# Optimization experiments

Hardware: AMD Instinct MI355X
Metric: run time of the kernel (lower is better)

Reference implementation:

```python
import jax, jax.numpy as jnp
import numpy as np

EPS = 1e-5

def _bn(x, g, b, m, v):
    # inference-mode batchnorm over channel axis 1
    s = (1, -1) + (1,) * (x.ndim - 2)
    return (x - m.reshape(s)) * (g.reshape(s) / jnp.sqrt(v.reshape(s) + EPS)) + b.reshape(s)

def _lrelu(x):
    return jnp.where(x >= 0, x, 0.2 * x)

def _graph_feature(x, k):
    # x: (B, C, N) -> (B, 2C, N, k): DGCNN cat([neighbor - center, center])
    xt = jnp.transpose(x, (0, 2, 1))                      # (B, N, C)
    sq = jnp.sum(xt * xt, axis=-1)                        # (B, N)
    neg_dist = 2.0 * jnp.einsum('bnc,bmc->bnm', xt, xt) - sq[:, :, None] - sq[:, None, :]
    idx = jax.lax.top_k(neg_dist, k)[1]                   # (B, N, k) nearest (incl. self)
    nb = jax.vmap(lambda f, i: f[i])(xt, idx)             # (B, N, k, C) neighbor gather
    ctr = jnp.broadcast_to(xt[:, :, None, :], nb.shape)
    feat = jnp.concatenate([nb - ctr, ctr], axis=-1)      # (B, N, k, 2C)
    return jnp.transpose(feat, (0, 3, 1, 2))

def _edge_conv(x, k, w, g, b, m, v):
    # 1x1 conv over edge features + BN + LeakyReLU(0.2) + max over k neighbors
    f = _graph_feature(x, k)
    h = jnp.einsum('oi,bink->bonk', w, f)
    return jnp.max(_lrelu(_bn(h, g, b, m, v)), axis=-1)   # (B, out, N)

def setup_inputs():
    key = jax.random.key(0)
    ks = jax.random.split(key, 40)
    rn = lambda i, s: jax.random.normal(ks[i], s, dtype=jnp.float32)
    ru = lambda i, s: jax.random.uniform(ks[i], s, dtype=jnp.float32)
    B, N, K = 8, 1024, 20
    inp = {'x': rn(0, (B, N, 3))}
    dims = [(64, 6), (64, 128), (128, 128), (256, 256)]
    for li, (o, ci) in enumerate(dims, 1):
        base = li * 5
        inp[f'c{li}w'] = rn(base, (o, ci)) * 0.2
        inp[f'c{li}g'] = ru(base + 1, (o,)) + 0.5
        inp[f'c{li}b'] = rn(base + 2, (o,)) * 0.1
        inp[f'c{li}m'] = rn(base + 3, (o,)) * 0.1
        inp[f'c{li}v'] = ru(base + 4, (o,)) + 0.5
    inp['f1w'] = rn(25, (128, 384)) * 0.05
    inp['f1b'] = rn(26, (128,)) * 0.1
    inp['n1g'] = ru(27, (128,)) + 0.5
    inp['n1b'] = rn(28, (128,)) * 0.1
    inp['n1m'] = rn(29, (128,)) * 0.1
    inp['n1v'] = ru(30, (128,)) + 0.5
    inp['f2w'] = rn(31, (16, 128)) * 0.1
    inp['f2b'] = rn(32, (16,)) * 0.1
    inp['n2g'] = ru(33, (16,)) + 0.5
    inp['n2b'] = rn(34, (16,)) * 0.1
    inp['n2m'] = rn(35, (16,)) * 0.1
    inp['n2v'] = ru(36, (16,)) + 0.5
    inp['f3w'] = rn(37, (1, 16)) * 0.2
    inp['f3b'] = rn(38, (1,)) * 0.1
    inp['k'] = K
    return inp

def reference(x, c1w, c1g, c1b, c1m, c1v, c2w, c2g, c2b, c2m, c2v,
              c3w, c3g, c3b, c3m, c3v, c4w, c4g, c4b, c4m, c4v,
              f1w, f1b, n1g, n1b, n1m, n1v, f2w, f2b, n2g, n2b, n2m, n2v,
              f3w, f3b, k):
    xt = jnp.transpose(x, (0, 2, 1))                       # (B, 3, N)
    h1 = _edge_conv(xt, k, c1w, c1g, c1b, c1m, c1v)        # (B, 64, N)
    h2 = _edge_conv(h1, k, c2w, c2g, c2b, c2m, c2v)        # (B, 64, N)
    h3 = _edge_conv(h2, k, c3w, c3g, c3b, c3m, c3v)        # (B, 128, N)
    h4 = _edge_conv(h3, k, c4w, c4g, c4b, c4m, c4v)        # (B, 256, N)
    p3 = jnp.max(h3, axis=-1)                              # global max pool over N
    p4 = jnp.max(h4, axis=-1)
    f = jnp.concatenate([p3, p4], axis=1)                  # (B, 384)
    f = jax.nn.relu(_bn(f @ f1w.T + f1b, n1g, n1b, n1m, n1v))
    f = jax.nn.relu(_bn(f @ f2w.T + f2b, n2g, n2b, n2m, n2v))
    return f @ f3w.T + f3b                                 # (B, 1)
```

## Files before the change

### kernel.cpp

```cpp
#include <hip/hip_runtime.h>
#include <math.h>

constexpr int B_ = 8;
constexpr int N_ = 1024;
constexpr int K_ = 20;
constexpr float EPS_ = 1e-5f;

typedef __attribute__((ext_vector_type(8))) short short8;
typedef __attribute__((ext_vector_type(4))) float f32x4;
typedef unsigned long long u64;

__device__ __forceinline__ void bf16split(float x, unsigned short& h, unsigned short& l) {
    unsigned u = __float_as_uint(x);
    unsigned rh = (u + 0x7FFFu + ((u >> 16) & 1u)) >> 16;
    h = (unsigned short)rh;
    float lof = x - __uint_as_float(rh << 16);
    unsigned ul = __float_as_uint(lof);
    l = (unsigned short)((ul + 0x7FFFu + ((ul >> 16) & 1u)) >> 16);
}

template <int C, int CP>
__global__ __launch_bounds__(256) void split_kernel(const float* __restrict__ h,
                                                    unsigned short* __restrict__ Hh,
                                                    unsigned short* __restrict__ Hl,
                                                    float* __restrict__ sq) {
    int p = blockIdx.x * 256 + threadIdx.x;
    if (p >= B_ * N_) return;
    const float* r = h + (size_t)p * C;
    unsigned short hb[CP], lb[CP];
    float s = 0.f;
#pragma unroll
    for (int c = 0; c < C; ++c) {
        float v = r[c];
        s += v * v;
        bf16split(v, hb[c], lb[c]);
    }
#pragma unroll
    for (int c = C; c < CP; ++c) { hb[c] = 0; lb[c] = 0; }
    sq[p] = s;
#pragma unroll
    for (int i = 0; i < CP / 8; ++i) {
        *(short8*)&Hh[(size_t)p * CP + 8 * i] = *(const short8*)&hb[8 * i];
        *(short8*)&Hl[(size_t)p * CP + 8 * i] = *(const short8*)&lb[8 * i];
    }
}

template <int CP>
__device__ __forceinline__ void distg_body(unsigned short* smem,
                                           const unsigned short* __restrict__ Hh,
                                           const unsigned short* __restrict__ Hl,
                                           const float* __restrict__ sq,
                                           float* __restrict__ dist, int bid) {
    constexpr int KC = CP / 32;
    constexpr int STR = 40;
    unsigned short* As = smem;
    unsigned short* Bs = smem + 2 * 128 * STR;
    int t = threadIdx.x;
    int bb = bid >> 6;
    int r0 = ((bid >> 3) & 7) * 128;
    int c0 = (bid & 7) * 128;
    size_t base = (size_t)bb * N_;
    int lane = t & 63, wave = t >> 6, quad = lane >> 4, nl = lane & 15;
    int wm = wave >> 1, wn = wave & 1;

    f32x4 acc[4][4];
#pragma unroll
    for (int mt = 0; mt < 4; ++mt)
#pragma unroll
        for (int nt = 0; nt < 4; ++nt) acc[mt][nt] = (f32x4){0.f, 0.f, 0.f, 0.f};

    for (int kc = 0; kc < KC; ++kc) {
        if (kc) __syncthreads();
#pragma unroll
        for (int i = 0; i < 2; ++i) {
            int cid = t + i * 256;
            int row = cid >> 2, j = cid & 3;
            size_t asrc = (base + r0 + row) * CP + kc * 32 + 8 * j;
            size_t bsrc = (base + c0 + row) * CP + kc * 32 + 8 * j;
            int dst = row * STR + 8 * j;
            *(short8*)&As[dst] = *(const short8*)&Hh[asrc];
            *(short8*)&As[128 * STR + dst] = *(const short8*)&Hl[asrc];
            *(short8*)&Bs[dst] = *(const short8*)&Hh[bsrc];
            *(short8*)&Bs[128 * STR + dst] = *(const short8*)&Hl[bsrc];
        }
        __syncthreads();
        short8 ah[4], al[4];
#pragma unroll
        for (int mt = 0; mt < 4; ++mt) {
            int off = (wm * 64 + mt * 16 + nl) * STR + quad * 8;
            ah[mt] = *(const short8*)&As[off];
            al[mt] = *(const short8*)&As[128 * STR + off];
        }
#pragma unroll
        for (int nt = 0; nt < 4; ++nt) {
            int off = (wn * 64 + nt * 16 + nl) * STR + quad * 8;
            short8 bh = *(const short8*)&Bs[off];
            short8 bl = *(const short8*)&Bs[128 * STR + off];
#pragma unroll
            for (int mt = 0; mt < 4; ++mt) {
                acc[mt][nt] = __builtin_amdgcn_mfma_f32_16x16x32_bf16(ah[mt], bh, acc[mt][nt], 0, 0, 0);
                acc[mt][nt] = __builtin_amdgcn_mfma_f32_16x16x32_bf16(ah[mt], bl, acc[mt][nt], 0, 0, 0);
                acc[mt][nt] = __builtin_amdgcn_mfma_f32_16x16x32_bf16(al[mt], bh, acc[mt][nt], 0, 0, 0);
            }
        }
    }
    float sqc[4];
#pragma unroll
    for (int nt = 0; nt < 4; ++nt) sqc[nt] = sq[base + c0 + wn * 64 + nt * 16 + nl];
    float* dbase = dist + (size_t)bb * N_ * N_;
#pragma unroll
    for (int mt = 0; mt < 4; ++mt) {
#pragma unroll
        for (int r = 0; r < 4; ++r) {
            int row = r0 + wm * 64 + mt * 16 + quad * 4 + r;
            float sqr = sq[base + row];
#pragma unroll
            for (int nt = 0; nt < 4; ++nt)
                dbase[(size_t)row * N_ + c0 + wn * 64 + nt * 16 + nl] =
                    2.f * acc[mt][nt][r] - sqr - sqc[nt];
        }
    }
}

template <int CP, int NOUT>
__device__ __forceinline__ void gemmyz_body(unsigned short* smem,
                                            const unsigned short* __restrict__ Hh,
                                            const unsigned short* __restrict__ Hl,
                                            const unsigned short* __restrict__ Wh,
                                            const unsigned short* __restrict__ Wl,
                                            const float* __restrict__ bias2,
                                            float* __restrict__ YZ, int yb) {
    constexpr int KC = CP / 32;
    constexpr int NTt = NOUT / 16;
    constexpr int STR = 40;
    unsigned short* As = smem;
    int t = threadIdx.x;
    int m0 = (yb & 63) * 128;
    int n0 = (yb >> 6) * 128;
    int lane = t & 63, wave = t >> 6, quad = lane >> 4, nl = lane & 15;
    int wm = wave >> 1, wn = wave & 1;

    f32x4 acc[4][4];
#pragma unroll
    for (int mt = 0; mt < 4; ++mt)
#pragma unroll
        for (int nt = 0; nt < 4; ++nt) acc[mt][nt] = (f32x4){0.f, 0.f, 0.f, 0.f};

    for (int kc = 0; kc < KC; ++kc) {
        if (kc) __syncthreads();
#pragma unroll
        for (int i = 0; i < 2; ++i) {
            int cid = t + i * 256;
            int row = cid >> 2, j = cid & 3;
            size_t src = ((size_t)(m0 + row)) * CP + kc * 32 + 8 * j;
            int dst = row * STR + 8 * j;
            *(short8*)&As[dst] = *(const short8*)&Hh[src];
            *(short8*)&As[128 * STR + dst] = *(const short8*)&Hl[src];
        }
        __syncthreads();
        short8 ah[4], al[4];
#pragma unroll
        for (int mt = 0; mt < 4; ++mt) {
            int off = (wm * 64 + mt * 16 + nl) * STR + quad * 8;
            ah[mt] = *(const short8*)&As[off];
            al[mt] = *(const short8*)&As[128 * STR + off];
        }
#pragma unroll
        for (int nt = 0; nt < 4; ++nt) {
            int ntg = (n0 >> 4) + wn * 4 + nt;
            size_t bpos = ((size_t)(kc * NTt + ntg) * 64 + lane) * 8;
            short8 bh = *(const short8*)&Wh[bpos];
            short8 bl = *(const short8*)&Wl[bpos];
#pragma unroll
            for (int mt = 0; mt < 4; ++mt) {
                acc[mt][nt] = __builtin_amdgcn_mfma_f32_16x16x32_bf16(ah[mt], bh, acc[mt][nt], 0, 0, 0);
                acc[mt][nt] = __builtin_amdgcn_mfma_f32_16x16x32_bf16(ah[mt], bl, acc[mt][nt], 0, 0, 0);
                acc[mt][nt] = __builtin_amdgcn_mfma_f32_16x16x32_bf16(al[mt], bh, acc[mt][nt], 0, 0, 0);
            }
        }
    }
#pragma unroll
    for (int nt = 0; nt < 4; ++nt) {
        int col = n0 + wn * 64 + nt * 16 + nl;
        float bv = bias2[col];
#pragma unroll
        for (int mt = 0; mt < 4; ++mt) {
#pragma unroll
            for (int r = 0; r < 4; ++r) {
                int row = m0 + wm * 64 + mt * 16 + quad * 4 + r;
                YZ[(size_t)row * NOUT + col] = acc[mt][nt][r] + bv;
            }
        }
    }
}

template <int CP>
__global__ __launch_bounds__(256) void distg_kernel(const unsigned short* __restrict__ Hh,
                                                    const unsigned short* __restrict__ Hl,
                                                    const float* __restrict__ sq,
                                                    float* __restrict__ dist) {
    __shared__ unsigned short smem[4 * 128 * 40];
    distg_body<CP>(smem, Hh, Hl, sq, dist, blockIdx.x);
}

template <int CP, int NOUT>
__global__ __launch_bounds__(256) void distyz_kernel(const unsigned short* __restrict__ Hh,
                                                     const unsigned short* __restrict__ Hl,
                                                     const float* __restrict__ sq,
                                                     float* __restrict__ dist,
                                                     const unsigned short* __restrict__ Wh,
                                                     const unsigned short* __restrict__ Wl,
                                                     const float* __restrict__ bias2,
                                                     float* __restrict__ YZ) {
    __shared__ unsigned short smem[4 * 128 * 40];
    if (blockIdx.x < 512)
        distg_body<CP>(smem, Hh, Hl, sq, dist, blockIdx.x);
    else
        gemmyz_body<CP, NOUT>(smem, Hh, Hl, Wh, Wl, bias2, YZ, blockIdx.x - 512);
}

__device__ __forceinline__ unsigned int fkey(float f) {
    unsigned int u = __float_as_uint(f);
    return (u & 0x80000000u) ? ~u : (u | 0x80000000u);
}

__device__ __forceinline__ u64 tree16(const u64* v) {
    u64 t0[8];
#pragma unroll
    for (int s = 0; s < 8; ++s) t0[s] = v[2 * s] > v[2 * s + 1] ? v[2 * s] : v[2 * s + 1];
#pragma unroll
    for (int s = 0; s < 4; ++s) t0[s] = t0[2 * s] > t0[2 * s + 1] ? t0[2 * s] : t0[2 * s + 1];
    t0[0] = t0[0] > t0[1] ? t0[0] : t0[1];
    t0[2] = t0[2] > t0[3] ? t0[2] : t0[3];
    return t0[0] > t0[2] ? t0[0] : t0[2];
}

__device__ __forceinline__ u64 wave_sort_desc(u64 v, int lane) {
#pragma unroll
    for (int k2 = 2; k2 <= 64; k2 <<= 1) {
#pragma unroll
        for (int j = k2 >> 1; j > 0; j >>= 1) {
            u64 o = __shfl_xor(v, j);
            bool desc = ((lane & k2) == 0);
            bool lower = ((lane & j) == 0);
            u64 mx = v > o ? v : o;
            u64 mn = v > o ? o : v;
            v = (desc == lower) ? mx : mn;
        }
    }
    return v;
}

__global__ __launch_bounds__(256) void sel_kernel(const float* __restrict__ dist,
                                                  int* __restrict__ idx) {
    __shared__ u64 cand[4][64];
    int t = threadIdx.x;
    int wave = t >> 6, lane = t & 63;
    int gr = blockIdx.x * 4 + wave;
    const float* d = dist + (size_t)gr * N_;
    int* op = idx + (size_t)gr * K_;
    int c0 = lane * 16;

    u64 kk[16];
#pragma unroll
    for (int i = 0; i < 4; ++i) {
        float4 a = *(const float4*)&d[c0 + 4 * i];
        float av[4] = {a.x, a.y, a.z, a.w};
#pragma unroll
        for (int e = 0; e < 4; ++e) {
            int c = c0 + 4 * i + e;
            kk[4 * i + e] = ((u64)fkey(av[e]) << 32) | (unsigned int)(~c);
        }
    }

    u64 lm = tree16(kk);
    u64 lms = wave_sort_desc(lm, lane);
    u64 tau = __shfl(lms, 19);

    int cnt = 0;
#pragma unroll
    for (int i = 0; i < 16; ++i) cnt += (kk[i] >= tau) ? 1 : 0;
    int incl = cnt;
#pragma unroll
    for (int dd = 1; dd < 64; dd <<= 1) {
        int n = __shfl_up(incl, dd);
        if (lane >= dd) incl += n;
    }
    int excl = incl - cnt;
    int Ctot = __shfl(incl, 63);

    if (Ctot <= 64) {
        cand[wave][lane] = 0ull;
        __builtin_amdgcn_wave_barrier();
        int pos = excl;
#pragma unroll
        for (int i = 0; i < 16; ++i) {
            if (kk[i] >= tau) { cand[wave][pos] = kk[i]; ++pos; }
        }
        __builtin_amdgcn_wave_barrier();
        u64 c = cand[wave][lane];
        c = wave_sort_desc(c, lane);
        if (lane < K_) op[lane] = (int)(~(unsigned int)c);
    } else {
        for (int it = 0; it < K_; ++it) {
            u64 m = tree16(kk);
#pragma unroll
            for (int off = 32; off; off >>= 1) {
                u64 o = __shfl_xor(m, off);
                m = o > m ? o : m;
            }
            if (lane == 0) op[it] = (int)(~(unsigned int)m);
#pragma unroll
            for (int j = 0; j < 16; ++j) kk[j] = (kk[j] == m) ? 0ull : kk[j];
        }
    }
}

__device__ __forceinline__ void prep_mfma2_elem(int e, int CIN, int COUT_,
                                                const float* w, const float* g,
                                                const float* bb, const float* m,
                                                const float* v,
                                                unsigned short* Wh, unsigned short* Wl,
                                                float* bias2) {
    int NOUT = 2 * COUT_;
    int NT = NOUT / 16;
    int n = e % NOUT, k = e / NOUT;
    int o = (n < COUT_) ? n : n - COUT_;
    float a = g[o] / sqrtf(v[o] + EPS_);
    float wv = (n < COUT_) ? a * w[o * 2 * CIN + k]
                           : a * (w[o * 2 * CIN + CIN + k] - w[o * 2 * CIN + k]);
    unsigned short hs, ls;
    bf16split(wv, hs, ls);
    int kc = k >> 5, ko = k & 31, quad = ko >> 3, j = ko & 7;
    int nt = n >> 4, nl = n & 15;
    size_t pos = ((size_t)(kc * NT + nt) * 64 + quad * 16 + nl) * 8 + j;
    Wh[pos] = hs;
    Wl[pos] = ls;
    if (k == 0) bias2[n] = (n < COUT_) ? 0.f : (bb[o] - m[o] * a);
}

__global__ __launch_bounds__(256) void prep_all(
    const float* __restrict__ w1, const float* __restrict__ g1, const float* __restrict__ bb1,
    const float* __restrict__ m1, const float* __restrict__ v1,
    const float* __restrict__ w2, const float* __restrict__ g2, const float* __restrict__ bb2,
    const float* __restrict__ m2, const float* __restrict__ v2,
    const float* __restrict__ w3, const float* __restrict__ g3, const float* __restrict__ bb3,
    const float* __restrict__ m3, const float* __restrict__ v3,
    const float* __restrict__ w4, const float* __restrict__ g4, const float* __restrict__ bb4,
    const float* __restrict__ m4, const float* __restrict__ v4,
    float* __restrict__ wd, float* __restrict__ wcd, float* __restrict__ bias1,
    unsigned short* __restrict__ Wh2, unsigned short* __restrict__ Wl2, float* __restrict__ b22,
    unsigned short* __restrict__ Wh3, unsigned short* __restrict__ Wl3, float* __restrict__ b23,
    unsigned short* __restrict__ Wh4, unsigned short* __restrict__ Wl4, float* __restrict__ b24) {
    int e = blockIdx.x * 256 + threadIdx.x;
    if (e < 192) {
        int o = e % 64, i = e / 64;
        float a = g1[o] / sqrtf(v1[o] + EPS_);
        float wdv = w1[o * 6 + i];
        wd[e] = a * wdv;
        wcd[e] = a * (w1[o * 6 + 3 + i] - wdv);
        if (i == 0) bias1[o] = bb1[o] - m1[o] * a;
    } else if (e < 192 + 8192) {
        prep_mfma2_elem(e - 192, 64, 64, w2, g2, bb2, m2, v2, Wh2, Wl2, b22);
    } else if (e < 192 + 8192 + 16384) {
        prep_mfma2_elem(e - 8384, 64, 128, w3, g3, bb3, m3, v3, Wh3, Wl3, b23);
    } else if (e < 192 + 8192 + 16384 + 65536) {
        prep_mfma2_elem(e - 24768, 128, 256, w4, g4, bb4, m4, v4, Wh4, Wl4, b24);
    }
}

__global__ __launch_bounds__(256) void y1z1_kernel(const float* __restrict__ x,
                                                   const float* __restrict__ wdT,
                                                   const float* __restrict__ wcdT,
                                                   const float* __restrict__ bias2,
                                                   float* __restrict__ YZ) {
    int t = threadIdx.x;
    int p = blockIdx.x * 4 + (t >> 6);
    int o = t & 63;
    float x0 = x[3 * p], x1 = x[3 * p + 1], x2 = x[3 * p + 2];
    float y = x0 * wdT[o] + x1 * wdT[64 + o] + x2 * wdT[128 + o];
    float z = bias2[o] + x0 * wcdT[o] + x1 * wcdT[64 + o] + x2 * wcdT[128 + o];
    YZ[(size_t)p * 128 + o] = y;
    YZ[(size_t)p * 128 + 64 + o] = z;
}

template <int COUT, bool WRITE_H>
__global__ __launch_bounds__(256) void gmxf_kernel(const float* __restrict__ YZ,
                                                   const int* __restrict__ idx,
                                                   unsigned short* __restrict__ Hh,
                                                   unsigned short* __restrict__ Hl,
                                                   float* __restrict__ sq,
                                                   float* __restrict__ h) {
    constexpr int NOUT = 2 * COUT;
    constexpr int PPG = 256 / COUT;
    __shared__ int nidx[PPG][K_];
    __shared__ float part[4];
    int t = threadIdx.x;
    int p0 = blockIdx.x * PPG;
    if (t < PPG * K_) nidx[t / K_][t % K_] = idx[(size_t)(p0 + t / K_) * K_ + t % K_];
    __syncthreads();
    int pg = t / COUT, o = t % COUT, p = p0 + pg;
    size_t ybase = (size_t)(p >> 10) << 10;
    float m = -INFINITY;
#pragma unroll
    for (int k = 0; k < K_; ++k)
        m = fmaxf(m, YZ[(ybase + nidx[pg][k]) * NOUT + o]);
    float val = m + YZ[(size_t)p * NOUT + COUT + o];
    val = (val >= 0.f) ? val : 0.2f * val;
    if constexpr (WRITE_H) h[(size_t)p * COUT + o] = val;
    unsigned short hi, lo;
    bf16split(val, hi, lo);
    Hh[(size_t)p * COUT + o] = hi;
    Hl[(size_t)p * COUT + o] = lo;
    float s = val * val;
#pragma unroll
    for (int d = 32; d; d >>= 1) s += __shfl_xor(s, d);
    int wave = t >> 6, lane = t & 63;
    if (lane == 0) part[wave] = s;
    __syncthreads();
    if (t < PPG) {
        constexpr int WPP = COUT / 64;
        float tot = 0.f;
#pragma unroll
        for (int w2 = 0; w2 < WPP; ++w2) tot += part[t * WPP + w2];
        sq[p0 + t] = tot;
    }
}

template <int COUT>
__global__ __launch_bounds__(256) void gathermax_kernel(const float* __restrict__ YZ,
                                                        const int* __restrict__ idx,
                                                        float* __restrict__ h) {
    constexpr int NOUT = 2 * COUT;
    constexpr int PPG = 256 / COUT;
    __shared__ int nidx[PPG][K_];
    int t = threadIdx.x;
    int p0 = blockIdx.x * PPG;
    if (t < PPG * K_) nidx[t / K_][t % K_] = idx[(size_t)(p0 + t / K_) * K_ + t % K_];
    __syncthreads();
    int pg = t / COUT;
    int o = t % COUT;
    int p = p0 + pg;
    size_t ybase = (size_t)(p >> 10) << 10;
    float m = -INFINITY;
#pragma unroll
    for (int k = 0; k < K_; ++k)
        m = fmaxf(m, YZ[(ybase + nidx[pg][k]) * NOUT + o]);
    float val = m + YZ[(size_t)p * NOUT + COUT + o];
    val = (val >= 0.f) ? val : 0.2f * val;
    h[(size_t)p * COUT + o] = val;
}

template <int C>
__global__ __launch_bounds__(256) void pool1_kernel(const float* __restrict__ h,
                                                    float* __restrict__ partial) {
    __shared__ float red[4][64];
    int bb = blockIdx.x, c0 = blockIdx.y * 64, z = blockIdx.z;
    int lane = threadIdx.x & 63, sl = threadIdx.x >> 6;
    int c = c0 + lane;
    const float* hb = h + (size_t)bb * N_ * C;
    int n0 = z * 64 + sl * 16;
    float mx = -INFINITY;
#pragma unroll
    for (int i = 0; i < 16; ++i) mx = fmaxf(mx, hb[(size_t)(n0 + i) * C + c]);
    red[sl][lane] = mx;
    __syncthreads();
    if (sl == 0) {
        mx = fmaxf(fmaxf(red[0][lane], red[1][lane]), fmaxf(red[2][lane], red[3][lane]));
        partial[((size_t)bb * 16 + z) * C + c] = mx;
    }
}

template <int C>
__global__ __launch_bounds__(64) void pool2_kernel(const float* __restrict__ partial,
                                                   float* __restrict__ f, int off) {
    int bb = blockIdx.x, c = blockIdx.y * 64 + threadIdx.x;
    float mx = -INFINITY;
#pragma unroll
    for (int z = 0; z < 16; ++z)
        mx = fmaxf(mx, partial[((size_t)bb * 16 + z) * C + c]);
    f[bb * 384 + off + c] = mx;
}

__global__ __launch_bounds__(128) void fc_tail(
    const float* __restrict__ f, const float* __restrict__ f1w,
    const float* __restrict__ f1b, const float* __restrict__ n1g,
    const float* __restrict__ n1b, const float* __restrict__ n1m,
    const float* __restrict__ n1v, const float* __restrict__ f2w,
    const float* __restrict__ f2b, const float* __restrict__ n2g,
    const float* __restrict__ n2b, const float* __restrict__ n2m,
    const float* __restrict__ n2v, const float* __restrict__ f3w,
    const float* __restrict__ f3b, float* __restrict__ out) {
    __shared__ float fb[384];
    __shared__ float s1[128];
    __shared__ float s2[16];
    int bb = blockIdx.x, t = threadIdx.x;
    for (int j = t; j < 384; j += 128) fb[j] = f[bb * 384 + j];
    __syncthreads();
    float a = f1b[t];
    for (int j = 0; j < 384; ++j) a += f1w[t * 384 + j] * fb[j];
    a = (a - n1m[t]) * (n1g[t] / sqrtf(n1v[t] + EPS_)) + n1b[t];
    s1[t] = fmaxf(a, 0.f);
    __syncthreads();
    if (t < 16) {
        float a2 = f2b[t];
        for (int j = 0; j < 128; ++j) a2 += f2w[t * 128 + j] * s1[j];
        a2 = (a2 - n2m[t]) * (n2g[t] / sqrtf(n2v[t] + EPS_)) + n2b[t];
        s2[t] = fmaxf(a2, 0.f);
    }
    __syncthreads();
    if (t == 0) {
        float a3 = f3b[0];
        for (int j = 0; j < 16; ++j) a3 += f3w[j] * s2[j];
        out[bb] = a3;
    }
}

extern "C" void kernel_launch(void* const* d_in, const int* in_sizes, int n_in,
                              void* d_out, int out_size, void* d_ws, size_t ws_size,
                              hipStream_t stream) {
    const float* x = (const float*)d_in[0];
    const float* cw[4] = {(const float*)d_in[1], (const float*)d_in[6],
                          (const float*)d_in[11], (const float*)d_in[16]};
    const float* cg[4] = {(const float*)d_in[2], (const float*)d_in[7],
                          (const float*)d_in[12], (const float*)d_in[17]};
    const float* cb[4] = {(const float*)d_in[3], (const float*)d_in[8],
                          (const float*)d_in[13], (const float*)d_in[18]};
    const float* cm[4] = {(const float*)d_in[4], (const float*)d_in[9],
                          (const float*)d_in[14], (const float*)d_in[19]};
    const float* cv[4] = {(const float*)d_in[5], (const float*)d_in[10],
                          (const float*)d_in[15], (const float*)d_in[20]};
    const float* f1w = (const float*)d_in[21];
    const float* f1b = (const float*)d_in[22];
    const float* n1g = (const float*)d_in[23];
    const float* n1b = (const float*)d_in[24];
    const float* n1m = (const float*)d_in[25];
    const float* n1v = (const float*)d_in[26];
    const float* f2w = (const float*)d_in[27];
    const float* f2b = (const float*)d_in[28];
    const float* n2g = (const float*)d_in[29];
    const float* n2b = (const float*)d_in[30];
    const float* n2m = (const float*)d_in[31];
    const float* n2v = (const float*)d_in[32];
    const float* f3w = (const float*)d_in[33];
    const float* f3b = (const float*)d_in[34];
    float* out = (float*)d_out;

    char* ws = (char*)d_ws;
    size_t off = 0;
    auto alloc = [&](size_t bytes) {
        void* p = ws + off;
        off += (bytes + 255) & ~(size_t)255;
        return p;
    };
    float* sq = (float*)alloc(B_ * N_ * 4);
    int* idx = (int*)alloc((size_t)B_ * N_ * K_ * 4);
    float* h3 = (float*)alloc((size_t)B_ * N_ * 128 * 4);
    float* h4 = (float*)alloc((size_t)B_ * N_ * 256 * 4);
    float* wd = (float*)alloc(3 * 64 * 4);
    float* wcd = (float*)alloc(3 * 64 * 4);
    float* bias1 = (float*)alloc(64 * 4);
    float* b22 = (float*)alloc(128 * 4);
    float* b23 = (float*)alloc(256 * 4);
    float* b24 = (float*)alloc(512 * 4);
    float* f = (float*)alloc(B_ * 384 * 4);
    float* partial = (float*)alloc((size_t)B_ * 16 * 256 * 4);
    unsigned short* Wh2 = (unsigned short*)alloc(64 * 128 * 2);
    unsigned short* Wl2 = (unsigned short*)alloc(64 * 128 * 2);
    unsigned short* Wh3 = (unsigned short*)alloc(64 * 256 * 2);
    unsigned short* Wl3 = (unsigned short*)alloc(64 * 256 * 2);
    unsigned short* Wh4 = (unsigned short*)alloc(128 * 512 * 2);
    unsigned short* Wl4 = (unsigned short*)alloc(128 * 512 * 2);
    unsigned short* Hh = (unsigned short*)alloc((size_t)B_ * N_ * 128 * 2);
    unsigned short* Hl = (unsigned short*)alloc((size_t)B_ * N_ * 128 * 2);
    float* dist = (float*)alloc((size_t)B_ * N_ * N_ * 4);
    float* YZ = (float*)alloc((size_t)B_ * N_ * 512 * 4);
    (void)ws_size; (void)in_sizes; (void)n_in; (void)out_size;

    const int SELG = B_ * (N_ / 4);
    const int SG = (B_ * N_) / 256;
    const int GM = B_ * N_;

    prep_all<<<(192 + 8192 + 16384 + 65536 + 255) / 256, 256, 0, stream>>>(
        cw[0], cg[0], cb[0], cm[0], cv[0], cw[1], cg[1], cb[1], cm[1], cv[1],
        cw[2], cg[2], cb[2], cm[2], cv[2], cw[3], cg[3], cb[3], cm[3], cv[3],
        wd, wcd, bias1, Wh2, Wl2, b22, Wh3, Wl3, b23, Wh4, Wl4, b24);

    split_kernel<3, 32><<<SG, 256, 0, stream>>>(x, Hh, Hl, sq);
    distg_kernel<32><<<B_ * 64, 256, 0, stream>>>(Hh, Hl, sq, dist);
    sel_kernel<<<SELG, 256, 0, stream>>>(dist, idx);
    y1z1_kernel<<<GM / 4, 256, 0, stream>>>(x, wd, wcd, bias1, YZ);
    gmxf_kernel<64, false><<<GM / 4, 256, 0, stream>>>(YZ, idx, Hh, Hl, sq, nullptr);

    distyz_kernel<64, 128><<<512 + 64, 256, 0, stream>>>(Hh, Hl, sq, dist, Wh2, Wl2, b22, YZ);
    sel_kernel<<<SELG, 256, 0, stream>>>(dist, idx);
    gmxf_kernel<64, false><<<GM / 4, 256, 0, stream>>>(YZ, idx, Hh, Hl, sq, nullptr);

    distyz_kernel<64, 256><<<512 + 128, 256, 0, stream>>>(Hh, Hl, sq, dist, Wh3, Wl3, b23, YZ);
    sel_kernel<<<SELG, 256, 0, stream>>>(dist, idx);
    gmxf_kernel<128, true><<<GM / 2, 256, 0, stream>>>(YZ, idx, Hh, Hl, sq, h3);

    distyz_kernel<128, 512><<<512 + 256, 256, 0, stream>>>(Hh, Hl, sq, dist, Wh4, Wl4, b24, YZ);
    sel_kernel<<<SELG, 256, 0, stream>>>(dist, idx);
    gathermax_kernel<256><<<GM, 256, 0, stream>>>(YZ, idx, h4);

    pool1_kernel<128><<<dim3(B_, 2, 16), 256, 0, stream>>>(h3, partial);
    pool2_kernel<128><<<dim3(B_, 2), 64, 0, stream>>>(partial, f, 0);
    pool1_kernel<256><<<dim3(B_, 4, 16), 256, 0, stream>>>(h4, partial);
    pool2_kernel<256><<<dim3(B_, 4), 64, 0, stream>>>(partial, f, 128);
    fc_tail<<<B_, 128, 0, stream>>>(f, f1w, f1b, n1g, n1b, n1m, n1v, f2w, f2b, n2g, n2b,
                                    n2m, n2v, f3w, f3b, out);
}
```

Measured before the change: 297.3 us.

## Fuse top-k selection into gather-max and merge small setup/pool launches

Measured after the change: 284.8 us. 1.04x faster.

```diff
diff --git a/kernel.cpp b/kernel.cpp
--- a/kernel.cpp
+++ b/kernel.cpp
@@ -17,32 +17,6 @@
     float lof = x - __uint_as_float(rh << 16);
     unsigned ul = __float_as_uint(lof);
     l = (unsigned short)((ul + 0x7FFFu + ((ul >> 16) & 1u)) >> 16);
-}
-
-template <int C, int CP>
-__global__ __launch_bounds__(256) void split_kernel(const float* __restrict__ h,
-                                                    unsigned short* __restrict__ Hh,
-                                                    unsigned short* __restrict__ Hl,
-                                                    float* __restrict__ sq) {
-    int p = blockIdx.x * 256 + threadIdx.x;
-    if (p >= B_ * N_) return;
-    const float* r = h + (size_t)p * C;
-    unsigned short hb[CP], lb[CP];
-    float s = 0.f;
-#pragma unroll
-    for (int c = 0; c < C; ++c) {
-        float v = r[c];
-        s += v * v;
-        bf16split(v, hb[c], lb[c]);
-    }
-#pragma unroll
-    for (int c = C; c < CP; ++c) { hb[c] = 0; lb[c] = 0; }
-    sq[p] = s;
-#pragma unroll
-    for (int i = 0; i < CP / 8; ++i) {
-        *(short8*)&Hh[(size_t)p * CP + 8 * i] = *(const short8*)&hb[8 * i];
-        *(short8*)&Hl[(size_t)p * CP + 8 * i] = *(const short8*)&lb[8 * i];
-    }
 }
 
 template <int CP>
@@ -194,15 +168,6 @@
     }
 }
 
-template <int CP>
-__global__ __launch_bounds__(256) void distg_kernel(const unsigned short* __restrict__ Hh,
-                                                    const unsigned short* __restrict__ Hl,
-                                                    const float* __restrict__ sq,
-                                                    float* __restrict__ dist) {
-    __shared__ unsigned short smem[4 * 128 * 40];
-    distg_body<CP>(smem, Hh, Hl, sq, dist, blockIdx.x);
-}
-
 template <int CP, int NOUT>
 __global__ __launch_bounds__(256) void distyz_kernel(const unsigned short* __restrict__ Hh,
                                                      const unsigned short* __restrict__ Hl,
@@ -219,6 +184,30 @@
         gemmyz_body<CP, NOUT>(smem, Hh, Hl, Wh, Wl, bias2, YZ, blockIdx.x - 512);
 }
 
+__global__ __launch_bounds__(256) void dist1y_kernel(const unsigned short* __restrict__ Hh,
+                                                     const unsigned short* __restrict__ Hl,
+                                                     const float* __restrict__ sq,
+                                                     float* __restrict__ dist,
+                                                     const float* __restrict__ x,
+                                                     const float* __restrict__ wdT,
+                                                     const float* __restrict__ wcdT,
+                                                     const float* __restrict__ bias1,
+                                                     float* __restrict__ YZ) {
+    __shared__ unsigned short smem[4 * 128 * 40];
+    if (blockIdx.x < 512) {
+        distg_body<32>(smem, Hh, Hl, sq, dist, blockIdx.x);
+    } else {
+        int t = threadIdx.x;
+        int p = (blockIdx.x - 512) * 4 + (t >> 6);
+        int o = t & 63;
+        float x0 = x[3 * p], x1 = x[3 * p + 1], x2 = x[3 * p + 2];
+        float y = x0 * wdT[o] + x1 * wdT[64 + o] + x2 * wdT[128 + o];
+        float z = bias1[o] + x0 * wcdT[o] + x1 * wcdT[64 + o] + x2 * wcdT[128 + o];
+        YZ[(size_t)p * 128 + o] = y;
+        YZ[(size_t)p * 128 + 64 + o] = z;
+    }
+}
+
 __device__ __forceinline__ unsigned int fkey(float f) {
     unsigned int u = __float_as_uint(f);
     return (u & 0x80000000u) ? ~u : (u | 0x80000000u);
@@ -251,16 +240,9 @@
     return v;
 }
 
-__global__ __launch_bounds__(256) void sel_kernel(const float* __restrict__ dist,
-                                                  int* __restrict__ idx) {
-    __shared__ u64 cand[4][64];
-    int t = threadIdx.x;
-    int wave = t >> 6, lane = t & 63;
-    int gr = blockIdx.x * 4 + wave;
-    const float* d = dist + (size_t)gr * N_;
-    int* op = idx + (size_t)gr * K_;
+__device__ __forceinline__ void sel_row(const float* __restrict__ d, int* nidxrow,
+                                        u64* candbuf, int lane) {
     int c0 = lane * 16;
-
     u64 kk[16];
 #pragma unroll
     for (int i = 0; i < 4; ++i) {
@@ -272,7 +254,6 @@
             kk[4 * i + e] = ((u64)fkey(av[e]) << 32) | (unsigned int)(~c);
         }
     }
-
     u64 lm = tree16(kk);
     u64 lms = wave_sort_desc(lm, lane);
     u64 tau = __shfl(lms, 19);
@@ -290,17 +271,17 @@
     int Ctot = __shfl(incl, 63);
 
     if (Ctot <= 64) {
-        cand[wave][lane] = 0ull;
+        candbuf[lane] = 0ull;
         __builtin_amdgcn_wave_barrier();
         int pos = excl;
 #pragma unroll
         for (int i = 0; i < 16; ++i) {
-            if (kk[i] >= tau) { cand[wave][pos] = kk[i]; ++pos; }
+            if (kk[i] >= tau) { candbuf[pos] = kk[i]; ++pos; }
         }
         __builtin_amdgcn_wave_barrier();
-        u64 c = cand[wave][lane];
+        u64 c = candbuf[lane];
         c = wave_sort_desc(c, lane);
-        if (lane < K_) op[lane] = (int)(~(unsigned int)c);
+        if (lane < K_) nidxrow[lane] = (int)(~(unsigned int)c);
     } else {
         for (int it = 0; it < K_; ++it) {
             u64 m = tree16(kk);
@@ -309,9 +290,57 @@
                 u64 o = __shfl_xor(m, off);
                 m = o > m ? o : m;
             }
-            if (lane == 0) op[it] = (int)(~(unsigned int)m);
+            if (lane == 0) nidxrow[it] = (int)(~(unsigned int)m);
 #pragma unroll
             for (int j = 0; j < 16; ++j) kk[j] = (kk[j] == m) ? 0ull : kk[j];
+        }
+    }
+}
+
+template <int COUT, bool WRITE_H, bool WRITE_NEXT>
+__global__ __launch_bounds__(256) void selgmx_kernel(const float* __restrict__ dist,
+                                                     const float* __restrict__ YZ,
+                                                     unsigned short* __restrict__ Hh,
+                                                     unsigned short* __restrict__ Hl,
+                                                     float* __restrict__ sq,
+                                                     float* __restrict__ h) {
+    constexpr int NOUT = 2 * COUT;
+    constexpr int PPG = 256 / COUT;
+    __shared__ int nidx[PPG][K_];
+    __shared__ u64 cand[PPG][64];
+    __shared__ float part[4];
+    int t = threadIdx.x, wave = t >> 6, lane = t & 63;
+    int p0 = blockIdx.x * PPG;
+
+    if (wave < PPG)
+        sel_row(dist + (size_t)(p0 + wave) * N_, nidx[wave], cand[wave], lane);
+    __syncthreads();
+
+    int pg = t / COUT, o = t % COUT, p = p0 + pg;
+    size_t ybase = (size_t)(p >> 10) << 10;
+    float m = -INFINITY;
+#pragma unroll
+    for (int k = 0; k < K_; ++k)
+        m = fmaxf(m, YZ[(ybase + nidx[pg][k]) * NOUT + o]);
+    float val = m + YZ[(size_t)p * NOUT + COUT + o];
+    val = (val >= 0.f) ? val : 0.2f * val;
+    if constexpr (WRITE_H) h[(size_t)p * COUT + o] = val;
+    if constexpr (WRITE_NEXT) {
+        unsigned short hi, lo;
+        bf16split(val, hi, lo);
+        Hh[(size_t)p * COUT + o] = hi;
+        Hl[(size_t)p * COUT + o] = lo;
+        float s = val * val;
+#pragma unroll
+        for (int d = 32; d; d >>= 1) s += __shfl_xor(s, d);
+        if (lane == 0) part[wave] = s;
+        __syncthreads();
+        if (t < PPG) {
+            constexpr int WPP = COUT / 64;
+            float tot = 0.f;
+#pragma unroll
+            for (int w2 = 0; w2 < WPP; ++w2) tot += part[t * WPP + w2];
+            sq[p0 + t] = tot;
         }
     }
 }
@@ -339,7 +368,9 @@
     if (k == 0) bias2[n] = (n < COUT_) ? 0.f : (bb[o] - m[o] * a);
 }
 
-__global__ __launch_bounds__(256) void prep_all(
+__global__ __launch_bounds__(256) void setup_kernel(
+    const float* __restrict__ x, unsigned short* __restrict__ Hh,
+    unsigned short* __restrict__ Hl, float* __restrict__ sq,
     const float* __restrict__ w1, const float* __restrict__ g1, const float* __restrict__ bb1,
     const float* __restrict__ m1, const float* __restrict__ v1,
     const float* __restrict__ w2, const float* __restrict__ g2, const float* __restrict__ bb2,
@@ -352,7 +383,29 @@
     unsigned short* __restrict__ Wh2, unsigned short* __restrict__ Wl2, float* __restrict__ b22,
     unsigned short* __restrict__ Wh3, unsigned short* __restrict__ Wl3, float* __restrict__ b23,
     unsigned short* __restrict__ Wh4, unsigned short* __restrict__ Wl4, float* __restrict__ b24) {
-    int e = blockIdx.x * 256 + threadIdx.x;
+    int t = threadIdx.x;
+    if (blockIdx.x < 32) {
+        int p = blockIdx.x * 256 + t;
+        const float* r = x + (size_t)p * 3;
+        unsigned short hb[32], lb[32];
+        float s = 0.f;
+#pragma unroll
+        for (int c = 0; c < 3; ++c) {
+            float v = r[c];
+            s += v * v;
+            bf16split(v, hb[c], lb[c]);
+        }
+#pragma unroll
+        for (int c = 3; c < 32; ++c) { hb[c] = 0; lb[c] = 0; }
+        sq[p] = s;
+#pragma unroll
+        for (int i = 0; i < 4; ++i) {
+            *(short8*)&Hh[(size_t)p * 32 + 8 * i] = *(const short8*)&hb[8 * i];
+            *(short8*)&Hl[(size_t)p * 32 + 8 * i] = *(const short8*)&lb[8 * i];
+        }
+        return;
+    }
+    int e = (blockIdx.x - 32) * 256 + t;
     if (e < 192) {
         int o = e % 64, i = e / 64;
         float a = g1[o] / sqrtf(v1[o] + EPS_);
@@ -369,95 +422,25 @@
     }
 }
 
-__global__ __launch_bounds__(256) void y1z1_kernel(const float* __restrict__ x,
-                                                   const float* __restrict__ wdT,
-                                                   const float* __restrict__ wcdT,
-                                                   const float* __restrict__ bias2,
-                                                   float* __restrict__ YZ) {
-    int t = threadIdx.x;
-    int p = blockIdx.x * 4 + (t >> 6);
-    int o = t & 63;
-    float x0 = x[3 * p], x1 = x[3 * p + 1], x2 = x[3 * p + 2];
-    float y = x0 * wdT[o] + x1 * wdT[64 + o] + x2 * wdT[128 + o];
-    float z = bias2[o] + x0 * wcdT[o] + x1 * wcdT[64 + o] + x2 * wcdT[128 + o];
-    YZ[(size_t)p * 128 + o] = y;
-    YZ[(size_t)p * 128 + 64 + o] = z;
-}
-
-template <int COUT, bool WRITE_H>
-__global__ __launch_bounds__(256) void gmxf_kernel(const float* __restrict__ YZ,
-                                                   const int* __restrict__ idx,
-                                                   unsigned short* __restrict__ Hh,
-                                                   unsigned short* __restrict__ Hl,
-                                                   float* __restrict__ sq,
-                                                   float* __restrict__ h) {
-    constexpr int NOUT = 2 * COUT;
-    constexpr int PPG = 256 / COUT;
-    __shared__ int nidx[PPG][K_];
-    __shared__ float part[4];
-    int t = threadIdx.x;
-    int p0 = blockIdx.x * PPG;
-    if (t < PPG * K_) nidx[t / K_][t % K_] = idx[(size_t)(p0 + t / K_) * K_ + t % K_];
-    __syncthreads();
-    int pg = t / COUT, o = t % COUT, p = p0 + pg;
-    size_t ybase = (size_t)(p >> 10) << 10;
-    float m = -INFINITY;
-#pragma unroll
-    for (int k = 0; k < K_; ++k)
-        m = fmaxf(m, YZ[(ybase + nidx[pg][k]) * NOUT + o]);
-    float val = m + YZ[(size_t)p * NOUT + COUT + o];
-    val = (val >= 0.f) ? val : 0.2f * val;
-    if constexpr (WRITE_H) h[(size_t)p * COUT + o] = val;
-    unsigned short hi, lo;
-    bf16split(val, hi, lo);
-    Hh[(size_t)p * COUT + o] = hi;
-    Hl[(size_t)p * COUT + o] = lo;
-    float s = val * val;
-#pragma unroll
-    for (int d = 32; d; d >>= 1) s += __shfl_xor(s, d);
-    int wave = t >> 6, lane = t & 63;
-    if (lane == 0) part[wave] = s;
-    __syncthreads();
-    if (t < PPG) {
-        constexpr int WPP = COUT / 64;
-        float tot = 0.f;
-#pragma unroll
-        for (int w2 = 0; w2 < WPP; ++w2) tot += part[t * WPP + w2];
-        sq[p0 + t] = tot;
-    }
-}
-
-template <int COUT>
-__global__ __launch_bounds__(256) void gathermax_kernel(const float* __restrict__ YZ,
-                                                        const int* __restrict__ idx,
-                                                        float* __restrict__ h) {
-    constexpr int NOUT = 2 * COUT;
-    constexpr int PPG = 256 / COUT;
-    __shared__ int nidx[PPG][K_];
-    int t = threadIdx.x;
-    int p0 = blockIdx.x * PPG;
-    if (t < PPG * K_) nidx[t / K_][t % K_] = idx[(size_t)(p0 + t / K_) * K_ + t % K_];
-    __syncthreads();
-    int pg = t / COUT;
-    int o = t % COUT;
-    int p = p0 + pg;
-    size_t ybase = (size_t)(p >> 10) << 10;
-    float m = -INFINITY;
-#pragma unroll
-    for (int k = 0; k < K_; ++k)
-        m = fmaxf(m, YZ[(ybase + nidx[pg][k]) * NOUT + o]);
-    float val = m + YZ[(size_t)p * NOUT + COUT + o];
-    val = (val >= 0.f) ? val : 0.2f * val;
-    h[(size_t)p * COUT + o] = val;
-}
-
-template <int C>
-__global__ __launch_bounds__(256) void pool1_kernel(const float* __restrict__ h,
-                                                    float* __restrict__ partial) {
+__global__ __launch_bounds__(256) void pool1_all(const float* __restrict__ h3,
+                                                 const float* __restrict__ h4,
+                                                 float* __restrict__ p128,
+                                                 float* __restrict__ p256) {
     __shared__ float red[4][64];
-    int bb = blockIdx.x, c0 = blockIdx.y * 64, z = blockIdx.z;
+    int bid = blockIdx.x;
+    const float* h;
+    float* part;
+    int C, bb, cb, z;
+    if (bid < 256) {
+        z = bid & 15; cb = (bid >> 4) & 1; bb = bid >> 5;
+        C = 128; h = h3; part = p128;
+    } else {
+        int e = bid - 256;
+        z = e & 15; cb = (e >> 4) & 3; bb = e >> 6;
+        C = 256; h = h4; part = p256;
+    }
     int lane = threadIdx.x & 63, sl = threadIdx.x >> 6;
-    int c = c0 + lane;
+    int c = cb * 64 + lane;
     const float* hb = h + (size_t)bb * N_ * C;
     int n0 = z * 64 + sl * 16;
     float mx = -INFINITY;
@@ -467,18 +450,23 @@
     __syncthreads();
     if (sl == 0) {
         mx = fmaxf(fmaxf(red[0][lane], red[1][lane]), fmaxf(red[2][lane], red[3][lane]));
-        partial[((size_t)bb * 16 + z) * C + c] = mx;
-    }
-}
-
-template <int C>
-__global__ __launch_bounds__(64) void pool2_kernel(const float* __restrict__ partial,
-                                                   float* __restrict__ f, int off) {
-    int bb = blockIdx.x, c = blockIdx.y * 64 + threadIdx.x;
+        part[((size_t)bb * 16 + z) * C + c] = mx;
+    }
+}
+
+__global__ __launch_bounds__(64) void pool2_all(const float* __restrict__ p128,
+                                                const float* __restrict__ p256,
+                                                float* __restrict__ f) {
+    int bid = blockIdx.x;
+    const float* part;
+    int C, bb, cb, off;
+    if (bid < 16) { cb = bid & 1; bb = bid >> 1; C = 128; part = p128; off = 0; }
+    else { int e = bid - 16; cb = e & 3; bb = e >> 2; C = 256; part = p256; off = 128; }
+    int c = cb * 64 + threadIdx.x;
     float mx = -INFINITY;
 #pragma unroll
     for (int z = 0; z < 16; ++z)
-        mx = fmaxf(mx, partial[((size_t)bb * 16 + z) * C + c]);
+        mx = fmaxf(mx, part[((size_t)bb * 16 + z) * C + c]);
     f[bb * 384 + off + c] = mx;
 }
 
@@ -554,7 +542,6 @@
         return p;
     };
     float* sq = (float*)alloc(B_ * N_ * 4);
-    int* idx = (int*)alloc((size_t)B_ * N_ * K_ * 4);
     float* h3 = (float*)alloc((size_t)B_ * N_ * 128 * 4);
     float* h4 = (float*)alloc((size_t)B_ * N_ * 256 * 4);
     float* wd = (float*)alloc(3 * 64 * 4);
@@ -564,7 +551,8 @@
     float* b23 = (float*)alloc(256 * 4);
     float* b24 = (float*)alloc(512 * 4);
     float* f = (float*)alloc(B_ * 384 * 4);
-    float* partial = (float*)alloc((size_t)B_ * 16 * 256 * 4);
+    float* p128 = (float*)alloc((size_t)B_ * 16 * 128 * 4);
+    float* p256 = (float*)alloc((size_t)B_ * 16 * 256 * 4);
     unsigned short* Wh2 = (unsigned short*)alloc(64 * 128 * 2);
     unsigned short* Wl2 = (unsigned short*)alloc(64 * 128 * 2);
     unsigned short* Wh3 = (unsigned short*)alloc(64 * 256 * 2);
@@ -577,37 +565,26 @@
     float* YZ = (float*)alloc((size_t)B_ * N_ * 512 * 4);
     (void)ws_size; (void)in_sizes; (void)n_in; (void)out_size;
 
-    const int SELG = B_ * (N_ / 4);
-    const int SG = (B_ * N_) / 256;
-    const int GM = B_ * N_;
-
-    prep_all<<<(192 + 8192 + 16384 + 65536 + 255) / 256, 256, 0, stream>>>(
+    setup_kernel<<<32 + (192 + 8192 + 16384 + 65536 + 255) / 256, 256, 0, stream>>>(
+        x, Hh, Hl, sq,
         cw[0], cg[0], cb[0], cm[0], cv[0], cw[1], cg[1], cb[1], cm[1], cv[1],
         cw[2], cg[2], cb[2], cm[2], cv[2], cw[3], cg[3], cb[3], cm[3], cv[3],
         wd, wcd, bias1, Wh2, Wl2, b22, Wh3, Wl3, b23, Wh4, Wl4, b24);
 
-    split_kernel<3, 32><<<SG, 256, 0, stream>>>(x, Hh, Hl, sq);
-    distg_kernel<32><<<B_ * 64, 256, 0, stream>>>(Hh, Hl, sq, dist);
-    sel_kernel<<<SELG, 256, 0, stream>>>(dist, idx);
-    y1z1_kernel<<<GM / 4, 256, 0, stream>>>(x, wd, wcd, bias1, YZ);
-    gmxf_kernel<64, false><<<GM / 4, 256, 0, stream>>>(YZ, idx, Hh, Hl, sq, nullptr);
+    dist1y_kernel<<<512 + 2048, 256, 0, stream>>>(Hh, Hl, sq, dist, x, wd, wcd, bias1, YZ);
+    selgmx_kernel<64, false, true><<<B_ * N_ / 4, 256, 0, stream>>>(dist, YZ, Hh, Hl, sq, nullptr);
 
     distyz_kernel<64, 128><<<512 + 64, 256, 0, stream>>>(Hh, Hl, sq, dist, Wh2, Wl2, b22, YZ);
-    sel_kernel<<<SELG, 256, 0, stream>>>(dist, idx);
-    gmxf_kernel<64, false><<<GM / 4, 256, 0, stream>>>(YZ, idx, Hh, Hl, sq, nullptr);
+    selgmx_kernel<64, false, true><<<B_ * N_ / 4, 256, 0, stream>>>(dist, YZ, Hh, Hl, sq, nullptr);
 
     distyz_kernel<64, 256><<<512 + 128, 256, 0, stream>>>(Hh, Hl, sq, dist, Wh3, Wl3, b23, YZ);
-    sel_kernel<<<SELG, 256, 0, stream>>>(dist, idx);
-    gmxf_kernel<128, true><<<GM / 2, 256, 0, stream>>>(YZ, idx, Hh, Hl, sq, h3);
+    selgmx_kernel<128, true, true><<<B_ * N_ / 2, 256, 0, stream>>>(dist, YZ, Hh, Hl, sq, h3);
 
     distyz_kernel<128, 512><<<512 + 256, 256, 0, stream>>>(Hh, Hl, sq, dist, Wh4, Wl4, b24, YZ);
-    sel_kernel<<<SELG, 256, 0, stream>>>(dist, idx);
-    gathermax_kernel<256><<<GM, 256, 0, stream>>>(YZ, idx, h4);
-
-    pool1_kernel<128><<<dim3(B_, 2, 16), 256, 0, stream>>>(h3, partial);
-    pool2_kernel<128><<<dim3(B_, 2), 64, 0, stream>>>(partial, f, 0);
-    pool1_kernel<256><<<dim3(B_, 4, 16), 256, 0, stream>>>(h4, partial);
-    pool2_kernel<256><<<dim3(B_, 4), 64, 0, stream>>>(partial, f, 128);
+    selgmx_kernel<256, true, false><<<B_ * N_, 256, 0, stream>>>(dist, YZ, nullptr, nullptr, nullptr, h4);
+
+    pool1_all<<<256 + 512, 256, 0, stream>>>(h3, h4, p128, p256);
+    pool2_all<<<16 + 32, 64, 0, stream>>>(p128, p256, f);
     fc_tail<<<B_, 128, 0, stream>>>(f, f1w, f1b, n1g, n1b, n1m, n1v, f2w, f2b, n2g, n2b,
                                     n2m, n2v, f3w, f3b, out);
 }
```
